# Performance work log

Measured on AMD Instinct MI355X. Metric: run time of the kernel, lower is better.

## Reference

```python
import jax, jax.numpy as jnp
import numpy as np

N_NODES = 50000
N_EDGES = 500000
IN_CH = 128
OUT_CH = 5
DIMS = [(IN_CH, 256), (256, 128), (128, 64)]
EPS = 1e-12  # F.normalize eps


def _lin_init(key, fan_out, fan_in):
    return jax.random.normal(key, (fan_out, fan_in), dtype=jnp.float32) * (1.0 / np.sqrt(fan_in))


def setup_inputs() -> dict:
    key = jax.random.key(0)
    ks = jax.random.split(key, 16)
    inp = {
        "x": jax.random.normal(ks[0], (N_NODES, IN_CH), dtype=jnp.float32),
        "edge_index": jax.random.randint(ks[1], (2, N_EDGES), 0, N_NODES, dtype=jnp.int64),
    }
    # SAGEConv params: lin_l (aggregated neighbors, with bias), lin_r (root, no bias)
    for i, (fi, fo) in enumerate(DIMS, start=1):
        inp[f"W{i}l"] = _lin_init(ks[3 * i], fo, fi)
        inp[f"b{i}"] = jnp.zeros((fo,), dtype=jnp.float32)
        inp[f"W{i}r"] = _lin_init(ks[3 * i + 1], fo, fi)
    inp["fcW"] = _lin_init(ks[13], OUT_CH, N_NODES * 64)
    inp["fcb"] = jnp.zeros((OUT_CH,), dtype=jnp.float32)
    return inp


def _sage(x, src, dst, Wl, bl, Wr):
    """PyG SAGEConv, aggr='mean', normalize=True: L2norm(lin_l(mean_j x_j) + lin_r(x_i))."""
    n = x.shape[0]
    agg = jax.ops.segment_sum(x[src], dst, num_segments=n)            # [N, F_in]
    deg = jax.ops.segment_sum(jnp.ones_like(src, dtype=x.dtype), dst, num_segments=n)
    mean = agg / jnp.clip(deg, 1.0)[:, None]
    out = mean @ Wl.T + bl + x @ Wr.T                                  # [N, F_out]
    nrm = jnp.linalg.norm(out, axis=-1, keepdims=True)
    return out / jnp.maximum(nrm, EPS)


def reference(x, edge_index, W1l, b1, W1r, W2l, b2, W2r, W3l, b3, W3r, fcW, fcb):
    src, dst = edge_index[0], edge_index[1]
    h = jax.nn.relu(_sage(x, src, dst, W1l, b1, W1r))
    h = jax.nn.relu(_sage(h, src, dst, W2l, b2, W2r))
    h = jax.nn.relu(_sage(h, src, dst, W3l, b3, W3r))
    logits = fcW @ h.reshape(-1) + fcb                                 # [OUT_CH]
    return jax.nn.softmax(logits, axis=-1)
```

## Files before the change

### kernel.cpp

```cpp
#include <hip/hip_runtime.h>
#include <hip/hip_bf16.h>
#include <math.h>

#define N_NODES 50000
#define N_EDGES 500000
#define FC_BLOCKS 1024

typedef __bf16 bf16x8 __attribute__((ext_vector_type(8)));
typedef float f32x4 __attribute__((ext_vector_type(4)));
typedef unsigned int u32x4 __attribute__((ext_vector_type(4)));

static __device__ __forceinline__ float bf2f_lo(unsigned int v) {
  return __uint_as_float(v << 16);
}
static __device__ __forceinline__ float bf2f_hi(unsigned int v) {
  return __uint_as_float(v & 0xffff0000u);
}
static __device__ __forceinline__ unsigned short f2bf(float f) {
  unsigned int u = __float_as_uint(f);
  return (unsigned short)((u + 0x7fffu + ((u >> 16) & 1u)) >> 16);
}
static __device__ __forceinline__ bf16x8 ld8(const unsigned short* p) {
  u32x4 u = *(const u32x4*)p;
  return __builtin_bit_cast(bf16x8, u);
}

__global__ void hist_kernel(const int* __restrict__ dst, int* __restrict__ cnt) {
  int e = blockIdx.x * blockDim.x + threadIdx.x;
  if (e < N_EDGES) atomicAdd(&cnt[dst[e]], 1);
}

__global__ void chunk_sum_kernel(const int* __restrict__ cnt, int* __restrict__ bsum) {
  __shared__ int s[512];
  int i = blockIdx.x * 512 + threadIdx.x;
  s[threadIdx.x] = (i < N_NODES) ? cnt[i] : 0;
  __syncthreads();
  for (int off = 256; off > 0; off >>= 1) {
    if (threadIdx.x < off) s[threadIdx.x] += s[threadIdx.x + off];
    __syncthreads();
  }
  if (threadIdx.x == 0) bsum[blockIdx.x] = s[0];
}

__global__ void scan_bsum_kernel(int* __restrict__ bsum, int n) {
  if (blockIdx.x == 0 && threadIdx.x == 0) {
    int acc = 0;
    for (int i = 0; i < n; i++) { int v = bsum[i]; bsum[i] = acc; acc += v; }
  }
}

__global__ void scan_final_kernel(const int* __restrict__ cnt, const int* __restrict__ bsum,
                                  int* __restrict__ row_ptr, float* __restrict__ inv_deg) {
  __shared__ int s[512];
  int i = blockIdx.x * 512 + threadIdx.x;
  int v = (i < N_NODES) ? cnt[i] : 0;
  s[threadIdx.x] = v;
  __syncthreads();
  for (int off = 1; off < 512; off <<= 1) {
    int t = (threadIdx.x >= off) ? s[threadIdx.x - off] : 0;
    __syncthreads();
    s[threadIdx.x] += t;
    __syncthreads();
  }
  if (i < N_NODES) {
    row_ptr[i + 1] = bsum[blockIdx.x] + s[threadIdx.x];
    if (i == 0) row_ptr[0] = 0;
    inv_deg[i] = 1.0f / fmaxf((float)v, 1.0f);
  }
}

__global__ void fill_csr_kernel(const int* __restrict__ src, const int* __restrict__ dst,
                                const int* __restrict__ row_ptr, int* __restrict__ fill,
                                int* __restrict__ col) {
  int e = blockIdx.x * blockDim.x + threadIdx.x;
  if (e < N_EDGES) {
    int d = dst[e];
    int pos = row_ptr[d] + atomicAdd(&fill[d], 1);
    col[pos] = src[e];
  }
}

__global__ void f2b_kernel(const float* __restrict__ in, unsigned short* __restrict__ out, int n4) {
  int i = blockIdx.x * 256 + threadIdx.x;
  if (i < n4) {
    float4 v = ((const float4*)in)[i];
    ushort4 o;
    o.x = f2bf(v.x); o.y = f2bf(v.y); o.z = f2bf(v.z); o.w = f2bf(v.w);
    ((ushort4*)out)[i] = o;
  }
}

__global__ void pack_kcat_kernel(const float* __restrict__ Wl, const float* __restrict__ Wr,
                                 unsigned short* __restrict__ Wt, int FIh, int FO) {
  int idx = blockIdx.x * 256 + threadIdx.x;
  int FI = 2 * FIh;
  if (idx < FI * FO) {
    int j = idx / FI, k = idx % FI;
    float v = (k < FIh) ? Wl[j * FIh + k] : Wr[j * FIh + (k - FIh)];
    Wt[idx] = f2bf(v);
  }
}

__global__ void pack_jcat_kernel(const float* __restrict__ Wl, const float* __restrict__ Wr,
                                 unsigned short* __restrict__ Wt, int FI, int FOh) {
  int idx = blockIdx.x * 256 + threadIdx.x;
  if (idx < 2 * FOh * FI) {
    int j = idx / FI, k = idx % FI;
    float v = (j < FOh) ? Wl[j * FI + k] : Wr[(j - FOh) * FI + k];
    Wt[idx] = f2bf(v);
  }
}

#define ACC8(v)                                          \
  do {                                                   \
    a[0] += bf2f_lo((v)[0]); a[1] += bf2f_hi((v)[0]);    \
    a[2] += bf2f_lo((v)[1]); a[3] += bf2f_hi((v)[1]);    \
    a[4] += bf2f_lo((v)[2]); a[5] += bf2f_hi((v)[2]);    \
    a[6] += bf2f_lo((v)[3]); a[7] += bf2f_hi((v)[3]);    \
  } while (0)

__global__ void agg_mean_bf16(const unsigned short* __restrict__ xb, const int* __restrict__ rp,
                              const int* __restrict__ cl, const float* __restrict__ idg,
                              unsigned short* __restrict__ out) {
  int node = blockIdx.x * 4 + (threadIdx.x >> 6);
  int lane = threadIdx.x & 63;
  int g = lane >> 4, l = lane & 15;
  int beg = rp[node], end = rp[node + 1];
  float a[8] = {0.f, 0.f, 0.f, 0.f, 0.f, 0.f, 0.f, 0.f};
  for (int e0 = beg; e0 < end; e0 += 8) {
    int e1 = e0 + g, e2 = e0 + 4 + g;
    if (e1 < end) {
      u32x4 v = *(const u32x4*)(xb + (size_t)cl[e1] * 128 + l * 8);
      ACC8(v);
    }
    if (e2 < end) {
      u32x4 v = *(const u32x4*)(xb + (size_t)cl[e2] * 128 + l * 8);
      ACC8(v);
    }
  }
  #pragma unroll
  for (int i = 0; i < 8; i++) {
    a[i] += __shfl_xor(a[i], 16);
    a[i] += __shfl_xor(a[i], 32);
  }
  if (g == 0) {
    float s = idg[node];
    u32x4 o;
    #pragma unroll
    for (int i = 0; i < 4; i++)
      o[i] = (unsigned int)f2bf(a[2 * i] * s) | ((unsigned int)f2bf(a[2 * i + 1] * s) << 16);
    *(u32x4*)(out + (size_t)node * 128 + l * 8) = o;
  }
}

__global__ void agg_nr128(const unsigned short* __restrict__ yl, const unsigned short* __restrict__ yr,
                          const float* __restrict__ bias, const int* __restrict__ rp,
                          const int* __restrict__ cl, const float* __restrict__ idg,
                          unsigned short* __restrict__ outb) {
  int node = blockIdx.x * 4 + (threadIdx.x >> 6);
  int lane = threadIdx.x & 63;
  int g = lane >> 4, l = lane & 15;
  int beg = rp[node], end = rp[node + 1];
  float a[8] = {0.f, 0.f, 0.f, 0.f, 0.f, 0.f, 0.f, 0.f};
  for (int e0 = beg; e0 < end; e0 += 8) {
    int e1 = e0 + g, e2 = e0 + 4 + g;
    if (e1 < end) {
      u32x4 v = *(const u32x4*)(yl + (size_t)cl[e1] * 128 + l * 8);
      ACC8(v);
    }
    if (e2 < end) {
      u32x4 v = *(const u32x4*)(yl + (size_t)cl[e2] * 128 + l * 8);
      ACC8(v);
    }
  }
  #pragma unroll
  for (int i = 0; i < 8; i++) {
    a[i] += __shfl_xor(a[i], 16);
    a[i] += __shfl_xor(a[i], 32);
  }
  float s = idg[node];
  u32x4 r = *(const u32x4*)(yr + (size_t)node * 128 + l * 8);
  float v[8];
  v[0] = a[0] * s + bias[l * 8 + 0] + bf2f_lo(r[0]);
  v[1] = a[1] * s + bias[l * 8 + 1] + bf2f_hi(r[0]);
  v[2] = a[2] * s + bias[l * 8 + 2] + bf2f_lo(r[1]);
  v[3] = a[3] * s + bias[l * 8 + 3] + bf2f_hi(r[1]);
  v[4] = a[4] * s + bias[l * 8 + 4] + bf2f_lo(r[2]);
  v[5] = a[5] * s + bias[l * 8 + 5] + bf2f_hi(r[2]);
  v[6] = a[6] * s + bias[l * 8 + 6] + bf2f_lo(r[3]);
  v[7] = a[7] * s + bias[l * 8 + 7] + bf2f_hi(r[3]);
  float p = 0.f;
  #pragma unroll
  for (int i = 0; i < 8; i++) p += v[i] * v[i];
  #pragma unroll
  for (int msk = 1; msk <= 8; msk <<= 1) p += __shfl_xor(p, msk);
  float sc = 1.0f / fmaxf(sqrtf(p), 1e-12f);
  if (g == 0) {
    u32x4 o;
    #pragma unroll
    for (int i = 0; i < 4; i++) {
      float w0 = fmaxf(v[2 * i] * sc, 0.f);
      float w1 = fmaxf(v[2 * i + 1] * sc, 0.f);
      o[i] = (unsigned int)f2bf(w0) | ((unsigned int)f2bf(w1) << 16);
    }
    *(u32x4*)(outb + (size_t)node * 128 + l * 8) = o;
  }
}

__global__ void agg_nr64(const unsigned short* __restrict__ yl, const unsigned short* __restrict__ yr,
                         const float* __restrict__ bias, const int* __restrict__ rp,
                         const int* __restrict__ cl, const float* __restrict__ idg,
                         float* __restrict__ outf) {
  int node = blockIdx.x * 4 + (threadIdx.x >> 6);
  int lane = threadIdx.x & 63;
  int g = lane >> 3, l = lane & 7;
  int beg = rp[node], end = rp[node + 1];
  float a[8] = {0.f, 0.f, 0.f, 0.f, 0.f, 0.f, 0.f, 0.f};
  for (int e0 = beg; e0 < end; e0 += 16) {
    int e1 = e0 + g, e2 = e0 + 8 + g;
    if (e1 < end) {
      u32x4 v = *(const u32x4*)(yl + (size_t)cl[e1] * 64 + l * 8);
      ACC8(v);
    }
    if (e2 < end) {
      u32x4 v = *(const u32x4*)(yl + (size_t)cl[e2] * 64 + l * 8);
      ACC8(v);
    }
  }
  #pragma unroll
  for (int i = 0; i < 8; i++) {
    a[i] += __shfl_xor(a[i], 8);
    a[i] += __shfl_xor(a[i], 16);
    a[i] += __shfl_xor(a[i], 32);
  }
  float s = idg[node];
  u32x4 r = *(const u32x4*)(yr + (size_t)node * 64 + l * 8);
  float v[8];
  v[0] = a[0] * s + bias[l * 8 + 0] + bf2f_lo(r[0]);
  v[1] = a[1] * s + bias[l * 8 + 1] + bf2f_hi(r[0]);
  v[2] = a[2] * s + bias[l * 8 + 2] + bf2f_lo(r[1]);
  v[3] = a[3] * s + bias[l * 8 + 3] + bf2f_hi(r[1]);
  v[4] = a[4] * s + bias[l * 8 + 4] + bf2f_lo(r[2]);
  v[5] = a[5] * s + bias[l * 8 + 5] + bf2f_hi(r[2]);
  v[6] = a[6] * s + bias[l * 8 + 6] + bf2f_lo(r[3]);
  v[7] = a[7] * s + bias[l * 8 + 7] + bf2f_hi(r[3]);
  float p = 0.f;
  #pragma unroll
  for (int i = 0; i < 8; i++) p += v[i] * v[i];
  #pragma unroll
  for (int msk = 1; msk <= 4; msk <<= 1) p += __shfl_xor(p, msk);
  float sc = 1.0f / fmaxf(sqrtf(p), 1e-12f);
  if (g == 0) {
    f32x4 o0, o1;
    #pragma unroll
    for (int i = 0; i < 4; i++) o0[i] = fmaxf(v[i] * sc, 0.f);
    #pragma unroll
    for (int i = 0; i < 4; i++) o1[i] = fmaxf(v[4 + i] * sc, 0.f);
    *(f32x4*)(outf + (size_t)node * 64 + l * 8) = o0;
    *(f32x4*)(outf + (size_t)node * 64 + l * 8 + 4) = o1;
  }
}

template<int FI, int FO, bool ASPLIT, bool POST, bool OSPLIT>
__launch_bounds__(256)
__global__ void mfma_gemm(const unsigned short* __restrict__ A1, const unsigned short* __restrict__ A2,
                          const unsigned short* __restrict__ W, const float* __restrict__ bias,
                          unsigned short* __restrict__ outA, unsigned short* __restrict__ outB) {
  constexpr int ROWB = FI * 2;
  constexpr int JF = FO / 64;
  __shared__ unsigned char As[64 * ROWB];
  __shared__ float sums[64][5];
  const int tid = threadIdx.x;
  const int wave = tid >> 6, lane = tid & 63;
  const int l15 = lane & 15, kg = lane >> 4;
  const int row0 = blockIdx.x * 64;
  const int wj = wave * (FO / 4);

  #pragma unroll
  for (int i = 0; i < (64 * ROWB) / 4096; i++) {
    int boff = i * 4096 + tid * 16;
    int row = boff / ROWB;
    int colb = boff % ROWB;
    int grow = row0 + row; if (grow >= N_NODES) grow = N_NODES - 1;
    u32x4 v;
    if (ASPLIT) {
      if (colb < ROWB / 2) v = *(const u32x4*)((const char*)A1 + (size_t)grow * (ROWB / 2) + colb);
      else                 v = *(const u32x4*)((const char*)A2 + (size_t)grow * (ROWB / 2) + colb - ROWB / 2);
    } else {
      v = *(const u32x4*)((const char*)A1 + (size_t)grow * ROWB + colb);
    }
    *(u32x4*)(&As[row * ROWB + (colb ^ ((row & 7) << 4))]) = v;
  }

  f32x4 acc[JF][4];
  #pragma unroll
  for (int jf = 0; jf < JF; jf++)
    #pragma unroll
    for (int mf = 0; mf < 4; mf++) acc[jf][mf] = (f32x4){0.f, 0.f, 0.f, 0.f};

  const unsigned short* Wp = W + (size_t)(wj + l15) * FI + kg * 8;
  bf16x8 wc[JF], wn[JF];
  #pragma unroll
  for (int jf = 0; jf < JF; jf++) wc[jf] = ld8(Wp + (size_t)jf * 16 * FI);

  __syncthreads();

  #pragma unroll
  for (int k0 = 0; k0 < FI; k0 += 32) {
    if (k0 + 32 < FI) {
      #pragma unroll
      for (int jf = 0; jf < JF; jf++) wn[jf] = ld8(Wp + (size_t)jf * 16 * FI + k0 + 32);
    }
    bf16x8 af[4];
    int colb = (k0 + kg * 8) * 2;
    #pragma unroll
    for (int mf = 0; mf < 4; mf++) {
      int row = mf * 16 + l15;
      af[mf] = ld8((const unsigned short*)&As[row * ROWB + (colb ^ ((row & 7) << 4))]);
    }
    #pragma unroll
    for (int jf = 0; jf < JF; jf++)
      #pragma unroll
      for (int mf = 0; mf < 4; mf++)
        acc[jf][mf] = __builtin_amdgcn_mfma_f32_16x16x32_bf16(wc[jf], af[mf], acc[jf][mf], 0, 0, 0);
    if (k0 + 32 < FI) {
      #pragma unroll
      for (int jf = 0; jf < JF; jf++) wc[jf] = wn[jf];
    }
  }

  if (POST) {
    float bj[JF][4];
    #pragma unroll
    for (int jf = 0; jf < JF; jf++)
      #pragma unroll
      for (int r = 0; r < 4; r++) bj[jf][r] = bias[wj + jf * 16 + kg * 4 + r];
    float p[4] = {0.f, 0.f, 0.f, 0.f};
    #pragma unroll
    for (int jf = 0; jf < JF; jf++)
      #pragma unroll
      for (int mf = 0; mf < 4; mf++)
        #pragma unroll
        for (int r = 0; r < 4; r++) {
          float v = acc[jf][mf][r] + bj[jf][r];
          acc[jf][mf][r] = v;
          p[mf] += v * v;
        }
    #pragma unroll
    for (int mf = 0; mf < 4; mf++) {
      p[mf] += __shfl_xor(p[mf], 16);
      p[mf] += __shfl_xor(p[mf], 32);
    }
    if (kg == 0) {
      #pragma unroll
      for (int mf = 0; mf < 4; mf++) sums[mf * 16 + l15][wave] = p[mf];
    }
    __syncthreads();
    #pragma unroll
    for (int mf = 0; mf < 4; mf++) {
      int rl = mf * 16 + l15;
      float tot = sums[rl][0] + sums[rl][1] + sums[rl][2] + sums[rl][3];
      float sc = 1.0f / fmaxf(sqrtf(tot), 1e-12f);
      #pragma unroll
      for (int jf = 0; jf < JF; jf++)
        #pragma unroll
        for (int r = 0; r < 4; r++) acc[jf][mf][r] = fmaxf(acc[jf][mf][r] * sc, 0.f);
    }
  }

  unsigned short* ob = outA;
  int cb = wj;
  constexpr int OSTR = OSPLIT ? FO / 2 : FO;
  if (OSPLIT && wj >= FO / 2) { ob = outB; cb = wj - FO / 2; }
  #pragma unroll
  for (int mf = 0; mf < 4; mf++) {
    int m = row0 + mf * 16 + l15;
    if (m < N_NODES) {
      #pragma unroll
      for (int jf = 0; jf < JF; jf++) {
        ushort4 o;
        o.x = f2bf(acc[jf][mf][0]);
        o.y = f2bf(acc[jf][mf][1]);
        o.z = f2bf(acc[jf][mf][2]);
        o.w = f2bf(acc[jf][mf][3]);
        *(ushort4*)&ob[(size_t)m * OSTR + cb + jf * 16 + kg * 4] = o;
      }
    }
  }
}

__global__ void fc_partial_kernel(const float* __restrict__ fcW, const float* __restrict__ h3,
                                  float* __restrict__ partial) {
  const size_t L = (size_t)N_NODES * 64;
  float acc[5] = {0.f, 0.f, 0.f, 0.f, 0.f};
  for (size_t i = (size_t)blockIdx.x * 256 + threadIdx.x; i < L; i += (size_t)gridDim.x * 256) {
    float h = h3[i];
    #pragma unroll
    for (int c = 0; c < 5; c++) acc[c] += h * fcW[(size_t)c * L + i];
  }
  __shared__ float red[4][5];
  #pragma unroll
  for (int msk = 1; msk <= 32; msk <<= 1)
    #pragma unroll
    for (int c = 0; c < 5; c++) acc[c] += __shfl_xor(acc[c], msk);
  int lane = threadIdx.x & 63, wave = threadIdx.x >> 6;
  if (lane == 0)
    #pragma unroll
    for (int c = 0; c < 5; c++) red[wave][c] = acc[c];
  __syncthreads();
  if (threadIdx.x < 5) {
    float s = red[0][threadIdx.x] + red[1][threadIdx.x] + red[2][threadIdx.x] + red[3][threadIdx.x];
    partial[blockIdx.x * 5 + threadIdx.x] = s;
  }
}

__global__ void fc_final_kernel(const float* __restrict__ partial, const float* __restrict__ fcb,
                                float* __restrict__ out) {
  __shared__ float red[4];
  __shared__ float logits[5];
  int tid = threadIdx.x;
  for (int c = 0; c < 5; c++) {
    float a = 0.f;
    for (int b = tid; b < FC_BLOCKS; b += 256) a += partial[b * 5 + c];
    #pragma unroll
    for (int msk = 1; msk <= 32; msk <<= 1) a += __shfl_xor(a, msk);
    if ((tid & 63) == 0) red[tid >> 6] = a;
    __syncthreads();
    if (tid == 0) logits[c] = red[0] + red[1] + red[2] + red[3] + fcb[c];
    __syncthreads();
  }
  if (tid == 0) {
    float mx = logits[0];
    for (int c = 1; c < 5; c++) mx = fmaxf(mx, logits[c]);
    float e[5], s = 0.f;
    for (int c = 0; c < 5; c++) { e[c] = expf(logits[c] - mx); s += e[c]; }
    for (int c = 0; c < 5; c++) out[c] = e[c] / s;
  }
}

extern "C" void kernel_launch(void* const* d_in, const int* in_sizes, int n_in,
                              void* d_out, int out_size, void* d_ws, size_t ws_size,
                              hipStream_t stream) {
  (void)in_sizes; (void)n_in; (void)out_size; (void)ws_size;
  const float* x   = (const float*)d_in[0];
  const int*   ei  = (const int*)d_in[1];
  const float* W1l = (const float*)d_in[2];
  const float* b1  = (const float*)d_in[3];
  const float* W1r = (const float*)d_in[4];
  const float* W2l = (const float*)d_in[5];
  const float* b2  = (const float*)d_in[6];
  const float* W2r = (const float*)d_in[7];
  const float* W3l = (const float*)d_in[8];
  const float* b3  = (const float*)d_in[9];
  const float* W3r = (const float*)d_in[10];
  const float* fcW = (const float*)d_in[11];
  const float* fcb = (const float*)d_in[12];
  const int* src = ei;
  const int* dst = ei + N_EDGES;

  char* ws = (char*)d_ws;
  size_t off = 0;
  auto alloc = [&](size_t bytes) { void* p = ws + off; off += (bytes + 255) & ~(size_t)255; return p; };
  int*   cnt     = (int*)alloc((size_t)N_NODES * 4);
  int*   row_ptr = (int*)alloc((size_t)(N_NODES + 1) * 4);
  int*   bsum    = (int*)alloc(512);
  float* inv_deg = (float*)alloc((size_t)N_NODES * 4);
  int*   col     = (int*)alloc((size_t)N_EDGES * 4);
  unsigned short* w1b = (unsigned short*)alloc((size_t)256 * 256 * 2);
  unsigned short* w2b = (unsigned short*)alloc((size_t)256 * 256 * 2);
  unsigned short* w3b = (unsigned short*)alloc((size_t)128 * 128 * 2);
  float* partial = (float*)alloc((size_t)FC_BLOCKS * 5 * 4);
  unsigned short* B0 = (unsigned short*)alloc((size_t)N_NODES * 128 * 2);
  unsigned short* B1 = (unsigned short*)alloc((size_t)N_NODES * 128 * 2);
  unsigned short* B2 = (unsigned short*)alloc((size_t)N_NODES * 256 * 2);
  unsigned short* B3 = (unsigned short*)alloc((size_t)N_NODES * 128 * 2);
  float* B4 = (float*)alloc((size_t)N_NODES * 64 * 4);
  float* out5 = (float*)d_out;

  unsigned short* xb    = B0;
  unsigned short* mean1 = B1;
  unsigned short* h1    = B2;
  unsigned short* y2l   = B1;
  unsigned short* y2r   = B0;
  unsigned short* h2    = B3;
  unsigned short* y3l   = B2;
  unsigned short* y3r   = B2 + (size_t)N_NODES * 64;
  float*          h3f   = B4;

  const int NCH = (N_NODES + 511) / 512;

  hipMemsetAsync(cnt, 0, (size_t)N_NODES * 4, stream);
  hist_kernel<<<(N_EDGES + 255) / 256, 256, 0, stream>>>(dst, cnt);
  chunk_sum_kernel<<<NCH, 512, 0, stream>>>(cnt, bsum);
  scan_bsum_kernel<<<1, 64, 0, stream>>>(bsum, NCH);
  scan_final_kernel<<<NCH, 512, 0, stream>>>(cnt, bsum, row_ptr, inv_deg);
  hipMemsetAsync(cnt, 0, (size_t)N_NODES * 4, stream);
  fill_csr_kernel<<<(N_EDGES + 255) / 256, 256, 0, stream>>>(src, dst, row_ptr, cnt, col);

  f2b_kernel<<<(N_NODES * 128 / 4 + 255) / 256, 256, 0, stream>>>(x, xb, N_NODES * 128 / 4);
  pack_kcat_kernel<<<(256 * 256 + 255) / 256, 256, 0, stream>>>(W1l, W1r, w1b, 128, 256);
  pack_jcat_kernel<<<(256 * 256 + 255) / 256, 256, 0, stream>>>(W2l, W2r, w2b, 256, 128);
  pack_jcat_kernel<<<(128 * 128 + 255) / 256, 256, 0, stream>>>(W3l, W3r, w3b, 128, 64);

  const int AGB = N_NODES / 4;
  const int GB  = (N_NODES + 63) / 64;

  agg_mean_bf16<<<AGB, 256, 0, stream>>>(xb, row_ptr, col, inv_deg, mean1);
  mfma_gemm<256, 256, true, true, false><<<GB, 256, 0, stream>>>(mean1, xb, w1b, b1, h1, nullptr);

  mfma_gemm<256, 256, false, false, true><<<GB, 256, 0, stream>>>(h1, nullptr, w2b, nullptr, y2l, y2r);
  agg_nr128<<<AGB, 256, 0, stream>>>(y2l, y2r, b2, row_ptr, col, inv_deg, h2);

  mfma_gemm<128, 128, false, false, true><<<GB, 256, 0, stream>>>(h2, nullptr, w3b, nullptr, y3l, y3r);
  agg_nr64<<<AGB, 256, 0, stream>>>(y3l, y3r, b3, row_ptr, col, inv_deg, h3f);

  fc_partial_kernel<<<FC_BLOCKS, 256, 0, stream>>>(fcW, h3f, partial);
  fc_final_kernel<<<1, 256, 0, stream>>>(partial, fcb, out5);
}
```

Baseline: 254.2 us.

## Fuse layer-1 and layer-2 GEMMs, merge prep kernels and single-block scan

Fuses the layer-1 GEMM with its normalize/ReLU epilogue and the layer-2 projection GEMM into one kernel. The normalized h1 tile is written back into shared memory and reused as the A operand, so the 50000x256 bf16 h1 buffer never round-trips through global memory. The x conversion, weight packing and counter zeroing are merged into one prep kernel, replacing several launches and memsets. The three-kernel scan becomes a single 1024-thread block scan, which saves launches but runs serially on one workgroup.

Result: slower. 318.5 us (+25.3%).

```diff
diff --git a/kernel.cpp b/kernel.cpp
--- a/kernel.cpp
+++ b/kernel.cpp
@@ -25,47 +25,70 @@
   return __builtin_bit_cast(bf16x8, u);
 }
 
+__global__ void prep_kernel(const float* __restrict__ x, unsigned short* __restrict__ xb,
+                            const float* __restrict__ W1l, const float* __restrict__ W1r,
+                            unsigned short* __restrict__ w1b,
+                            const float* __restrict__ W2l, const float* __restrict__ W2r,
+                            unsigned short* __restrict__ w2b,
+                            const float* __restrict__ W3l, const float* __restrict__ W3r,
+                            unsigned short* __restrict__ w3b,
+                            int* __restrict__ cntfill) {
+  int idx = blockIdx.x * 256 + threadIdx.x;
+  if (idx < 1600000) {
+    float4 v = ((const float4*)x)[idx];
+    ushort4 o;
+    o.x = f2bf(v.x); o.y = f2bf(v.y); o.z = f2bf(v.z); o.w = f2bf(v.w);
+    ((ushort4*)xb)[idx] = o;
+  } else if (idx < 1665536) {
+    int i = idx - 1600000;
+    int j = i >> 8, k = i & 255;
+    float v = (k < 128) ? W1l[j * 128 + k] : W1r[j * 128 + (k - 128)];
+    w1b[i] = f2bf(v);
+  } else if (idx < 1731072) {
+    int i = idx - 1665536;
+    int j = i >> 8, k = i & 255;
+    float v = (j < 128) ? W2l[j * 256 + k] : W2r[(j - 128) * 256 + k];
+    w2b[i] = f2bf(v);
+  } else if (idx < 1747456) {
+    int i = idx - 1731072;
+    int j = i >> 7, k = i & 127;
+    float v = (j < 64) ? W3l[j * 128 + k] : W3r[(j - 64) * 128 + k];
+    w3b[i] = f2bf(v);
+  } else if (idx < 1772456) {
+    int i = idx - 1747456;
+    ((int4*)cntfill)[i] = make_int4(0, 0, 0, 0);
+  }
+}
+
 __global__ void hist_kernel(const int* __restrict__ dst, int* __restrict__ cnt) {
   int e = blockIdx.x * blockDim.x + threadIdx.x;
   if (e < N_EDGES) atomicAdd(&cnt[dst[e]], 1);
 }
 
-__global__ void chunk_sum_kernel(const int* __restrict__ cnt, int* __restrict__ bsum) {
-  __shared__ int s[512];
-  int i = blockIdx.x * 512 + threadIdx.x;
-  s[threadIdx.x] = (i < N_NODES) ? cnt[i] : 0;
+__global__ void scan_kernel(const int* __restrict__ cnt, int* __restrict__ row_ptr,
+                            float* __restrict__ inv_deg) {
+  __shared__ int s[1024];
+  const int PER = 49;
+  int t = threadIdx.x;
+  int i0 = t * PER;
+  int i1 = i0 + PER; if (i1 > N_NODES) i1 = N_NODES;
+  int sum = 0;
+  for (int i = i0; i < i1; i++) sum += cnt[i];
+  s[t] = sum;
   __syncthreads();
-  for (int off = 256; off > 0; off >>= 1) {
-    if (threadIdx.x < off) s[threadIdx.x] += s[threadIdx.x + off];
+  for (int off = 1; off < 1024; off <<= 1) {
+    int v = (t >= off) ? s[t - off] : 0;
     __syncthreads();
-  }
-  if (threadIdx.x == 0) bsum[blockIdx.x] = s[0];
-}
-
-__global__ void scan_bsum_kernel(int* __restrict__ bsum, int n) {
-  if (blockIdx.x == 0 && threadIdx.x == 0) {
-    int acc = 0;
-    for (int i = 0; i < n; i++) { int v = bsum[i]; bsum[i] = acc; acc += v; }
-  }
-}
-
-__global__ void scan_final_kernel(const int* __restrict__ cnt, const int* __restrict__ bsum,
-                                  int* __restrict__ row_ptr, float* __restrict__ inv_deg) {
-  __shared__ int s[512];
-  int i = blockIdx.x * 512 + threadIdx.x;
-  int v = (i < N_NODES) ? cnt[i] : 0;
-  s[threadIdx.x] = v;
-  __syncthreads();
-  for (int off = 1; off < 512; off <<= 1) {
-    int t = (threadIdx.x >= off) ? s[threadIdx.x - off] : 0;
+    s[t] += v;
     __syncthreads();
-    s[threadIdx.x] += t;
-    __syncthreads();
-  }
-  if (i < N_NODES) {
-    row_ptr[i + 1] = bsum[blockIdx.x] + s[threadIdx.x];
-    if (i == 0) row_ptr[0] = 0;
-    inv_deg[i] = 1.0f / fmaxf((float)v, 1.0f);
+  }
+  int run = s[t] - sum;
+  if (t == 0) row_ptr[0] = 0;
+  for (int i = i0; i < i1; i++) {
+    int c = cnt[i];
+    run += c;
+    row_ptr[i + 1] = run;
+    inv_deg[i] = 1.0f / fmaxf((float)c, 1.0f);
   }
 }
 
@@ -77,37 +100,6 @@
     int d = dst[e];
     int pos = row_ptr[d] + atomicAdd(&fill[d], 1);
     col[pos] = src[e];
-  }
-}
-
-__global__ void f2b_kernel(const float* __restrict__ in, unsigned short* __restrict__ out, int n4) {
-  int i = blockIdx.x * 256 + threadIdx.x;
-  if (i < n4) {
-    float4 v = ((const float4*)in)[i];
-    ushort4 o;
-    o.x = f2bf(v.x); o.y = f2bf(v.y); o.z = f2bf(v.z); o.w = f2bf(v.w);
-    ((ushort4*)out)[i] = o;
-  }
-}
-
-__global__ void pack_kcat_kernel(const float* __restrict__ Wl, const float* __restrict__ Wr,
-                                 unsigned short* __restrict__ Wt, int FIh, int FO) {
-  int idx = blockIdx.x * 256 + threadIdx.x;
-  int FI = 2 * FIh;
-  if (idx < FI * FO) {
-    int j = idx / FI, k = idx % FI;
-    float v = (k < FIh) ? Wl[j * FIh + k] : Wr[j * FIh + (k - FIh)];
-    Wt[idx] = f2bf(v);
-  }
-}
-
-__global__ void pack_jcat_kernel(const float* __restrict__ Wl, const float* __restrict__ Wr,
-                                 unsigned short* __restrict__ Wt, int FI, int FOh) {
-  int idx = blockIdx.x * 256 + threadIdx.x;
-  if (idx < 2 * FOh * FI) {
-    int j = idx / FI, k = idx % FI;
-    float v = (j < FOh) ? Wl[j * FI + k] : Wr[(j - FOh) * FI + k];
-    Wt[idx] = f2bf(v);
   }
 }
 
@@ -261,6 +253,172 @@
   }
 }
 
+__launch_bounds__(256)
+__global__ void gemm12_kernel(const unsigned short* __restrict__ A1,
+                              const unsigned short* __restrict__ A2,
+                              const unsigned short* __restrict__ W1, const float* __restrict__ b1,
+                              const unsigned short* __restrict__ W2,
+                              unsigned short* __restrict__ y2l, unsigned short* __restrict__ y2r) {
+  __shared__ unsigned char As[64 * 512];
+  __shared__ float sums[64][5];
+  const int tid = threadIdx.x;
+  const int wave = tid >> 6, lane = tid & 63;
+  const int l15 = lane & 15, kg = lane >> 4;
+  const int row0 = blockIdx.x * 64;
+  const int wj = wave * 64;
+
+  #pragma unroll
+  for (int i = 0; i < 8; i++) {
+    int boff = i * 4096 + tid * 16;
+    int row = boff >> 9;
+    int colb = boff & 511;
+    int grow = row0 + row; if (grow >= N_NODES) grow = N_NODES - 1;
+    u32x4 v;
+    if (colb < 256) v = *(const u32x4*)((const char*)A1 + (size_t)grow * 256 + colb);
+    else            v = *(const u32x4*)((const char*)A2 + (size_t)grow * 256 + colb - 256);
+    *(u32x4*)(&As[row * 512 + (colb ^ ((row & 7) << 4))]) = v;
+  }
+
+  f32x4 acc[4][4];
+  #pragma unroll
+  for (int jf = 0; jf < 4; jf++)
+    #pragma unroll
+    for (int mf = 0; mf < 4; mf++) acc[jf][mf] = (f32x4){0.f, 0.f, 0.f, 0.f};
+
+  const unsigned short* Wp1 = W1 + (size_t)(wj + l15) * 256 + kg * 8;
+  bf16x8 wc[4], wn[4];
+  #pragma unroll
+  for (int jf = 0; jf < 4; jf++) wc[jf] = ld8(Wp1 + jf * 4096);
+
+  __syncthreads();
+
+  #pragma unroll
+  for (int k0 = 0; k0 < 256; k0 += 32) {
+    if (k0 < 224) {
+      #pragma unroll
+      for (int jf = 0; jf < 4; jf++) wn[jf] = ld8(Wp1 + jf * 4096 + k0 + 32);
+    }
+    bf16x8 af[4];
+    int colb = (k0 + kg * 8) * 2;
+    #pragma unroll
+    for (int mf = 0; mf < 4; mf++) {
+      int row = mf * 16 + l15;
+      af[mf] = ld8((const unsigned short*)&As[row * 512 + (colb ^ ((row & 7) << 4))]);
+    }
+    #pragma unroll
+    for (int jf = 0; jf < 4; jf++)
+      #pragma unroll
+      for (int mf = 0; mf < 4; mf++)
+        acc[jf][mf] = __builtin_amdgcn_mfma_f32_16x16x32_bf16(wc[jf], af[mf], acc[jf][mf], 0, 0, 0);
+    if (k0 < 224) {
+      #pragma unroll
+      for (int jf = 0; jf < 4; jf++) wc[jf] = wn[jf];
+    }
+  }
+
+  {
+    float p[4] = {0.f, 0.f, 0.f, 0.f};
+    #pragma unroll
+    for (int jf = 0; jf < 4; jf++)
+      #pragma unroll
+      for (int r = 0; r < 4; r++) {
+        float bj = b1[wj + jf * 16 + kg * 4 + r];
+        #pragma unroll
+        for (int mf = 0; mf < 4; mf++) {
+          float v = acc[jf][mf][r] + bj;
+          acc[jf][mf][r] = v;
+          p[mf] += v * v;
+        }
+      }
+    #pragma unroll
+    for (int mf = 0; mf < 4; mf++) {
+      p[mf] += __shfl_xor(p[mf], 16);
+      p[mf] += __shfl_xor(p[mf], 32);
+    }
+    if (kg == 0) {
+      #pragma unroll
+      for (int mf = 0; mf < 4; mf++) sums[mf * 16 + l15][wave] = p[mf];
+    }
+    __syncthreads();
+    #pragma unroll
+    for (int mf = 0; mf < 4; mf++) {
+      int rl = mf * 16 + l15;
+      float tot = sums[rl][0] + sums[rl][1] + sums[rl][2] + sums[rl][3];
+      float sc = 1.0f / fmaxf(sqrtf(tot), 1e-12f);
+      #pragma unroll
+      for (int jf = 0; jf < 4; jf++)
+        #pragma unroll
+        for (int r = 0; r < 4; r++) acc[jf][mf][r] = fmaxf(acc[jf][mf][r] * sc, 0.f);
+    }
+  }
+
+  #pragma unroll
+  for (int mf = 0; mf < 4; mf++) {
+    int row = mf * 16 + l15;
+    #pragma unroll
+    for (int jf = 0; jf < 4; jf++) {
+      ushort4 o;
+      o.x = f2bf(acc[jf][mf][0]);
+      o.y = f2bf(acc[jf][mf][1]);
+      o.z = f2bf(acc[jf][mf][2]);
+      o.w = f2bf(acc[jf][mf][3]);
+      int colb = (wj + jf * 16 + kg * 4) * 2;
+      *(ushort4*)(&As[row * 512 + (colb ^ ((row & 7) << 4))]) = o;
+    }
+  }
+  const unsigned short* Wp2 = W2 + (size_t)(wj + l15) * 256 + kg * 8;
+  #pragma unroll
+  for (int jf = 0; jf < 4; jf++) wc[jf] = ld8(Wp2 + jf * 4096);
+  #pragma unroll
+  for (int jf = 0; jf < 4; jf++)
+    #pragma unroll
+    for (int mf = 0; mf < 4; mf++) acc[jf][mf] = (f32x4){0.f, 0.f, 0.f, 0.f};
+
+  __syncthreads();
+
+  #pragma unroll
+  for (int k0 = 0; k0 < 256; k0 += 32) {
+    if (k0 < 224) {
+      #pragma unroll
+      for (int jf = 0; jf < 4; jf++) wn[jf] = ld8(Wp2 + jf * 4096 + k0 + 32);
+    }
+    bf16x8 af[4];
+    int colb = (k0 + kg * 8) * 2;
+    #pragma unroll
+    for (int mf = 0; mf < 4; mf++) {
+      int row = mf * 16 + l15;
+      af[mf] = ld8((const unsigned short*)&As[row * 512 + (colb ^ ((row & 7) << 4))]);
+    }
+    #pragma unroll
+    for (int jf = 0; jf < 4; jf++)
+      #pragma unroll
+      for (int mf = 0; mf < 4; mf++)
+        acc[jf][mf] = __builtin_amdgcn_mfma_f32_16x16x32_bf16(wc[jf], af[mf], acc[jf][mf], 0, 0, 0);
+    if (k0 < 224) {
+      #pragma unroll
+      for (int jf = 0; jf < 4; jf++) wc[jf] = wn[jf];
+    }
+  }
+
+  unsigned short* ob = (wj >= 128) ? y2r : y2l;
+  int cb = wj & 127;
+  #pragma unroll
+  for (int mf = 0; mf < 4; mf++) {
+    int m = row0 + mf * 16 + l15;
+    if (m < N_NODES) {
+      #pragma unroll
+      for (int jf = 0; jf < 4; jf++) {
+        ushort4 o;
+        o.x = f2bf(acc[jf][mf][0]);
+        o.y = f2bf(acc[jf][mf][1]);
+        o.z = f2bf(acc[jf][mf][2]);
+        o.w = f2bf(acc[jf][mf][3]);
+        *(ushort4*)&ob[(size_t)m * 128 + cb + jf * 16 + kg * 4] = o;
+      }
+    }
+  }
+}
+
 template<int FI, int FO, bool ASPLIT, bool POST, bool OSPLIT>
 __launch_bounds__(256)
 __global__ void mfma_gemm(const unsigned short* __restrict__ A1, const unsigned short* __restrict__ A2,
@@ -330,22 +488,19 @@
   }
 
   if (POST) {
-    float bj[JF][4];
+    float p[4] = {0.f, 0.f, 0.f, 0.f};
     #pragma unroll
     for (int jf = 0; jf < JF; jf++)
       #pragma unroll
-      for (int r = 0; r < 4; r++) bj[jf][r] = bias[wj + jf * 16 + kg * 4 + r];
-    float p[4] = {0.f, 0.f, 0.f, 0.f};
-    #pragma unroll
-    for (int jf = 0; jf < JF; jf++)
-      #pragma unroll
-      for (int mf = 0; mf < 4; mf++)
+      for (int r = 0; r < 4; r++) {
+        float bj = bias[wj + jf * 16 + kg * 4 + r];
         #pragma unroll
-        for (int r = 0; r < 4; r++) {
-          float v = acc[jf][mf][r] + bj[jf][r];
+        for (int mf = 0; mf < 4; mf++) {
+          float v = acc[jf][mf][r] + bj;
           acc[jf][mf][r] = v;
           p[mf] += v * v;
         }
+      }
     #pragma unroll
     for (int mf = 0; mf < 4; mf++) {
       p[mf] += __shfl_xor(p[mf], 16);
@@ -461,9 +616,8 @@
   char* ws = (char*)d_ws;
   size_t off = 0;
   auto alloc = [&](size_t bytes) { void* p = ws + off; off += (bytes + 255) & ~(size_t)255; return p; };
-  int*   cnt     = (int*)alloc((size_t)N_NODES * 4);
+  int*   cntfill = (int*)alloc((size_t)100000 * 4);
   int*   row_ptr = (int*)alloc((size_t)(N_NODES + 1) * 4);
-  int*   bsum    = (int*)alloc(512);
   float* inv_deg = (float*)alloc((size_t)N_NODES * 4);
   int*   col     = (int*)alloc((size_t)N_EDGES * 4);
   unsigned short* w1b = (unsigned short*)alloc((size_t)256 * 256 * 2);
@@ -477,9 +631,10 @@
   float* B4 = (float*)alloc((size_t)N_NODES * 64 * 4);
   float* out5 = (float*)d_out;
 
+  int*   cnt  = cntfill;
+  int*   fill = cntfill + N_NODES;
   unsigned short* xb    = B0;
   unsigned short* mean1 = B1;
-  unsigned short* h1    = B2;
   unsigned short* y2l   = B1;
   unsigned short* y2r   = B0;
   unsigned short* h2    = B3;
@@ -487,28 +642,18 @@
   unsigned short* y3r   = B2 + (size_t)N_NODES * 64;
   float*          h3f   = B4;
 
-  const int NCH = (N_NODES + 511) / 512;
-
-  hipMemsetAsync(cnt, 0, (size_t)N_NODES * 4, stream);
+  prep_kernel<<<(1772456 + 255) / 256, 256, 0, stream>>>(
+      x, xb, W1l, W1r, w1b, W2l, W2r, w2b, W3l, W3r, w3b, cntfill);
+
   hist_kernel<<<(N_EDGES + 255) / 256, 256, 0, stream>>>(dst, cnt);
-  chunk_sum_kernel<<<NCH, 512, 0, stream>>>(cnt, bsum);
-  scan_bsum_kernel<<<1, 64, 0, stream>>>(bsum, NCH);
-  scan_final_kernel<<<NCH, 512, 0, stream>>>(cnt, bsum, row_ptr, inv_deg);
-  hipMemsetAsync(cnt, 0, (size_t)N_NODES * 4, stream);
-  fill_csr_kernel<<<(N_EDGES + 255) / 256, 256, 0, stream>>>(src, dst, row_ptr, cnt, col);
-
-  f2b_kernel<<<(N_NODES * 128 / 4 + 255) / 256, 256, 0, stream>>>(x, xb, N_NODES * 128 / 4);
-  pack_kcat_kernel<<<(256 * 256 + 255) / 256, 256, 0, stream>>>(W1l, W1r, w1b, 128, 256);
-  pack_jcat_kernel<<<(256 * 256 + 255) / 256, 256, 0, stream>>>(W2l, W2r, w2b, 256, 128);
-  pack_jcat_kernel<<<(128 * 128 + 255) / 256, 256, 0, stream>>>(W3l, W3r, w3b, 128, 64);
+  scan_kernel<<<1, 1024, 0, stream>>>(cnt, row_ptr, inv_deg);
+  fill_csr_kernel<<<(N_EDGES + 255) / 256, 256, 0, stream>>>(src, dst, row_ptr, fill, col);
 
   const int AGB = N_NODES / 4;
   const int GB  = (N_NODES + 63) / 64;
 
   agg_mean_bf16<<<AGB, 256, 0, stream>>>(xb, row_ptr, col, inv_deg, mean1);
-  mfma_gemm<256, 256, true, true, false><<<GB, 256, 0, stream>>>(mean1, xb, w1b, b1, h1, nullptr);
-
-  mfma_gemm<256, 256, false, false, true><<<GB, 256, 0, stream>>>(h1, nullptr, w2b, nullptr, y2l, y2r);
+  gemm12_kernel<<<GB, 256, 0, stream>>>(mean1, xb, w1b, b1, w2b, y2l, y2r);
   agg_nr128<<<AGB, 256, 0, stream>>>(y2l, y2r, b2, row_ptr, col, inv_deg, h2);
 
   mfma_gemm<128, 128, false, false, true><<<GB, 256, 0, stream>>>(h2, nullptr, w3b, nullptr, y3l, y3r);
```
